# Kernel tuning notes

Hardware: AMD Instinct MI355X
Metric: run time of the kernel (lower is better)

Reference implementation:

```python
import jax, jax.numpy as jnp
import numpy as np

EPS = 1e-6
NUM_HEADS = 4


def setup_inputs() -> dict:
    key = jax.random.key(0)
    ks = jax.random.split(key, 7)
    B, C, H, W = 4, 128, 64, 64
    x = jax.random.normal(ks[0], (B, C, H, W), dtype=jnp.float32)
    norm_w = jnp.ones((C,), dtype=jnp.float32)
    norm_b = jnp.zeros((C,), dtype=jnp.float32)
    # 1x1 convs stored as [out_ch, in_ch] matrices
    qkv_w = jax.random.normal(ks[1], (3 * C, C), dtype=jnp.float32) / np.sqrt(C)
    qkv_b = jnp.zeros((3 * C,), dtype=jnp.float32)
    proj_w = jax.random.normal(ks[2], (C, C), dtype=jnp.float32) / np.sqrt(C)
    proj_b = jnp.zeros((C,), dtype=jnp.float32)
    return {"x": x, "norm_w": norm_w, "norm_b": norm_b,
            "qkv_w": qkv_w, "qkv_b": qkv_b, "proj_w": proj_w, "proj_b": proj_b}


def reference(x, norm_w, norm_b, qkv_w, qkv_b, proj_w, proj_b):
    B, C, H, W = x.shape
    nh = NUM_HEADS
    dh = C // nh
    N = H * W

    # ChannelLayerNorm: stats over channel dim per spatial position
    mean = jnp.mean(x, axis=1, keepdims=True)
    var = jnp.mean(jnp.square(x - mean), axis=1, keepdims=True)  # unbiased=False
    h = (x - mean) * jax.lax.rsqrt(var + EPS)
    h = h * norm_w[None, :, None, None] + norm_b[None, :, None, None]

    # qkv 1x1 conv -> [B, 3C, H, W]
    qkv = jnp.einsum('oc,bchw->bohw', qkv_w, h) + qkv_b[None, :, None, None]
    qkv = qkv.reshape(B, 3, nh, dh, N)
    q, k, v = qkv[:, 0], qkv[:, 1], qkv[:, 2]  # each [B, nh, dh, N]

    scale = dh ** -0.5
    attn = jnp.einsum('bhcn,bhcm->bhnm', q, k) * scale  # [B, nh, N, N]
    attn = jax.nn.softmax(attn, axis=-1)
    h = jnp.einsum('bhnm,bhcm->bhcn', attn, v)  # [B, nh, dh, N]
    h = h.reshape(B, C, H, W)

    h = jnp.einsum('oc,bchw->bohw', proj_w, h) + proj_b[None, :, None, None]
    return x + h
```

## Files before the change

kernel.cpp:

```cpp
#include <hip/hip_runtime.h>
#include <hip/hip_bf16.h>
#include <math.h>

#define BB 4
#define CC 128
#define NH 4
#define DH 32
#define NN 4096
#define OC3 (3*CC)

typedef __attribute__((ext_vector_type(8))) short short8;
typedef __attribute__((ext_vector_type(4))) short short4v;
typedef __attribute__((ext_vector_type(4))) float float4v;

__device__ inline short f2bf(float f) {
    unsigned u = __builtin_bit_cast(unsigned, f);
    u += 0x7FFF + ((u >> 16) & 1);
    return (short)(u >> 16);
}
__device__ inline unsigned pk2bf(float a, float b) {
    __hip_bfloat162 h = __float22bfloat162_rn(make_float2(a, b));
    unsigned u; __builtin_memcpy(&u, &h, 4);
    return u;
}
__device__ inline float bf2f(short s) {
    unsigned u = ((unsigned)(unsigned short)s) << 16;
    return __builtin_bit_cast(float, u);
}

#define HS 136
__global__ __launch_bounds__(512, 4) void lnqkv_kernel(
        const float* __restrict__ x, const float* __restrict__ nw,
        const float* __restrict__ nb, const float* __restrict__ qw,
        const float* __restrict__ qbias,
        short* __restrict__ qT, short* __restrict__ kT, short* __restrict__ vv) {
    __shared__ short hT[64 * HS];
    __shared__ float red[16][64];
    __shared__ float mrs[2][64];
    int t = threadIdx.x;
    int n0g = blockIdx.x * 64;
    int b = n0g >> 12, n0 = n0g & (NN - 1);
    int nl = t & 63, cq = t >> 6;

    const float* xp = x + ((size_t)b * CC + cq * 16) * NN + n0 + nl;
    float xv[16];
    float s = 0.f, ss = 0.f;
    #pragma unroll
    for (int j = 0; j < 16; ++j) {
        xv[j] = xp[(size_t)j * NN];
        s += xv[j]; ss += xv[j] * xv[j];
    }
    red[cq][nl] = s; red[cq + 8][nl] = ss;
    __syncthreads();
    if (t < 64) {
        float s8 = 0.f, q8 = 0.f;
        #pragma unroll
        for (int j = 0; j < 8; ++j) { s8 += red[j][t]; q8 += red[j + 8][t]; }
        float mean = s8 * (1.0f / CC);
        float var  = q8 * (1.0f / CC) - mean * mean;
        mrs[0][t] = mean;
        mrs[1][t] = rsqrtf(var + 1e-6f);
    }
    __syncthreads();
    {
        float mean = mrs[0][nl], rsv = mrs[1][nl];
        #pragma unroll
        for (int j = 0; j < 16; j += 8) {
            union { short8 v; unsigned u[4]; } z;
            #pragma unroll
            for (int k = 0; k < 4; ++k) {
                int c = cq * 16 + j + 2 * k;
                float h0 = (xv[j + 2 * k]     - mean) * rsv * nw[c]     + nb[c];
                float h1 = (xv[j + 2 * k + 1] - mean) * rsv * nw[c + 1] + nb[c + 1];
                z.u[k] = pk2bf(h0, h1);
            }
            *(short8*)&hT[nl * HS + cq * 16 + j] = z.v;
        }
    }
    __syncthreads();

    int w = t >> 6, lane = t & 63;
    int lg = lane >> 4, ln = lane & 15;
    int type = blockIdx.y;
    int ow = w * 16;
    const float* wp = qw + (size_t)(type * CC + ow + ln) * CC;
    float4v a0 = {0,0,0,0}, a1 = {0,0,0,0}, a2 = {0,0,0,0}, a3 = {0,0,0,0};
    #pragma unroll
    for (int cs = 0; cs < 4; ++cs) {
        float4 wa = *(const float4*)(wp + cs * 32 + lg * 8);
        float4 wb = *(const float4*)(wp + cs * 32 + lg * 8 + 4);
        union { short8 v; unsigned u[4]; } af;
        af.u[0] = pk2bf(wa.x, wa.y); af.u[1] = pk2bf(wa.z, wa.w);
        af.u[2] = pk2bf(wb.x, wb.y); af.u[3] = pk2bf(wb.z, wb.w);
        const short* hp = &hT[cs * 32 + lg * 8];
        a0 = __builtin_amdgcn_mfma_f32_16x16x32_bf16(af.v, *(const short8*)&hp[(0  + ln) * HS], a0, 0, 0, 0);
        a1 = __builtin_amdgcn_mfma_f32_16x16x32_bf16(af.v, *(const short8*)&hp[(16 + ln) * HS], a1, 0, 0, 0);
        a2 = __builtin_amdgcn_mfma_f32_16x16x32_bf16(af.v, *(const short8*)&hp[(32 + ln) * HS], a2, 0, 0, 0);
        a3 = __builtin_amdgcn_mfma_f32_16x16x32_bf16(af.v, *(const short8*)&hp[(48 + ln) * HS], a3, 0, 0, 0);
    }
    int r0g = type * CC + ow + lg * 4;
    float b0 = qbias[r0g], b1 = qbias[r0g + 1], b2 = qbias[r0g + 2], b3 = qbias[r0g + 3];
    int hh = ow >> 5;
    int cb = ow & 31;
    float4v* accs[4] = {&a0, &a1, &a2, &a3};
    if (type == 0) {
        const float qs = 0.1767766952966369f * 1.4426950408889634f;
        size_t rowbase = (size_t)(b * NH + hh) * NN + n0;
        #pragma unroll
        for (int nsub = 0; nsub < 4; ++nsub) {
            float4v av = *accs[nsub];
            union { short4v v; unsigned u[2]; } z;
            z.u[0] = pk2bf((av.x + b0) * qs, (av.y + b1) * qs);
            z.u[1] = pk2bf((av.z + b2) * qs, (av.w + b3) * qs);
            *(short4v*)&qT[(rowbase + nsub * 16 + ln) * DH + cb + lg * 4] = z.v;
        }
    } else if (type == 1) {
        size_t rowbase = (size_t)(b * NH + hh) * NN + n0;
        #pragma unroll
        for (int nsub = 0; nsub < 4; ++nsub) {
            float4v av = *accs[nsub];
            union { short4v v; unsigned u[2]; } z;
            z.u[0] = pk2bf(av.x + b0, av.y + b1);
            z.u[1] = pk2bf(av.z + b2, av.w + b3);
            *(short4v*)&kT[(rowbase + nsub * 16 + ln) * DH + cb + lg * 4] = z.v;
        }
    } else {
        size_t cbase = (size_t)((b * NH + hh) * DH + cb + lg * 4);
        #pragma unroll
        for (int nsub = 0; nsub < 4; ++nsub) {
            float4v av = *accs[nsub];
            size_t col = (size_t)n0 + nsub * 16 + ln;
            vv[(cbase + 0) * NN + col] = f2bf(av.x + b0);
            vv[(cbase + 1) * NN + col] = f2bf(av.y + b1);
            vv[(cbase + 2) * NN + col] = f2bf(av.z + b2);
            vv[(cbase + 3) * NN + col] = f2bf(av.w + b3);
        }
    }
}

#define PS 72
union __align__(16) FlashSh {
    short pt[8 * 4 * 16 * PS];
    struct { float mo[3][8][64][8]; float ml[3][8][64]; } m;
};
__global__ __launch_bounds__(512, 2) void flash_kernel(
        const short* __restrict__ qT, const short* __restrict__ kT,
        const short* __restrict__ vv, short* __restrict__ aoT) {
    __shared__ FlashSh sh;
    int blk = blockIdx.x;
    int bh = blk >> 5;
    int qb = blk & 31;
    int b = bh >> 2, hh = bh & 3;
    int n0 = qb * 128;
    int t = threadIdx.x, w = t >> 6, lane = t & 63;
    int lg = lane >> 4, ln = lane & 15;
    int qg = w & 1;
    int split = w >> 1;
    int swz = (ln & 3) << 2;

    const short* kbase = kT + (size_t)bh * NN * DH + lg * 8;
    const short* vb0 = vv + ((size_t)bh * DH + ln) * NN + lg * 8;
    const short* vb1 = vb0 + (size_t)16 * NN;

    short8 qf[4];
    #pragma unroll
    for (int j = 0; j < 4; ++j)
        qf[j] = *(const short8*)&qT[((size_t)bh * NN + n0 + (qg * 4 + j) * 16 + ln) * DH + lg * 8];

    float4v o0[4], o1[4];
    float ls[4];
    #pragma unroll
    for (int j = 0; j < 4; ++j) {
        o0[j] = (float4v){0,0,0,0}; o1[j] = (float4v){0,0,0,0}; ls[j] = 0.f;
    }
    short* ptw = &sh.pt[(w * 4) * 16 * PS];

    int mbeg = split * (NN / 4), mend = mbeg + NN / 4;
    for (int m0 = mbeg; m0 < mend; m0 += 64) {
        const short* kp = kbase + (size_t)m0 * DH;
        short8 k0 = *(const short8*)(kp + (size_t)(ln +  0) * DH);
        short8 k1 = *(const short8*)(kp + (size_t)(ln + 16) * DH);
        short8 k2 = *(const short8*)(kp + (size_t)(ln + 32) * DH);
        short8 k3 = *(const short8*)(kp + (size_t)(ln + 48) * DH);
        short8 v0 = *(const short8*)(vb0 + m0);
        short8 v1 = *(const short8*)(vb0 + m0 + 32);
        short8 v2 = *(const short8*)(vb1 + m0);
        short8 v3 = *(const short8*)(vb1 + m0 + 32);

        #pragma unroll
        for (int j = 0; j < 4; ++j) {
            float4v s0 = {0,0,0,0}, s1 = s0, s2 = s0, s3 = s0;
            s0 = __builtin_amdgcn_mfma_f32_16x16x32_bf16(k0, qf[j], s0, 0, 0, 0);
            s1 = __builtin_amdgcn_mfma_f32_16x16x32_bf16(k1, qf[j], s1, 0, 0, 0);
            s2 = __builtin_amdgcn_mfma_f32_16x16x32_bf16(k2, qf[j], s2, 0, 0, 0);
            s3 = __builtin_amdgcn_mfma_f32_16x16x32_bf16(k3, qf[j], s3, 0, 0, 0);
            short* ptj = ptw + j * 16 * PS;
            float lacc = 0.f;
            float4v* sv[4] = {&s0, &s1, &s2, &s3};
            #pragma unroll
            for (int jj = 0; jj < 4; ++jj) {
                float4v sj = *sv[jj];
                float p0 = __builtin_amdgcn_exp2f(sj.x);
                float p1 = __builtin_amdgcn_exp2f(sj.y);
                float p2 = __builtin_amdgcn_exp2f(sj.z);
                float p3 = __builtin_amdgcn_exp2f(sj.w);
                lacc += (p0 + p1) + (p2 + p3);
                union { short4v v; unsigned u[2]; } z;
                z.u[0] = pk2bf(p0, p1); z.u[1] = pk2bf(p2, p3);
                *(short4v*)&ptj[ln * PS + ((jj * 4 + lg) ^ swz) * 4] = z.v;
            }
            ls[j] += lacc;
        }

        #pragma unroll
        for (int j = 0; j < 4; ++j) {
            short* ptj = ptw + j * 16 * PS;
            short8 pb0 = *(const short8*)&ptj[ln * PS + ((2 * lg) ^ swz) * 4];
            short8 pb1 = *(const short8*)&ptj[ln * PS + ((8 + 2 * lg) ^ swz) * 4];
            o0[j] = __builtin_amdgcn_mfma_f32_16x16x32_bf16(v0, pb0, o0[j], 0, 0, 0);
            o1[j] = __builtin_amdgcn_mfma_f32_16x16x32_bf16(v2, pb0, o1[j], 0, 0, 0);
            o0[j] = __builtin_amdgcn_mfma_f32_16x16x32_bf16(v1, pb1, o0[j], 0, 0, 0);
            o1[j] = __builtin_amdgcn_mfma_f32_16x16x32_bf16(v3, pb1, o1[j], 0, 0, 0);
        }
    }

    __syncthreads();
    if (split > 0) {
        int si = split - 1;
        #pragma unroll
        for (int j = 0; j < 4; ++j) {
            int tid = qg * 4 + j;
            float* mp = &sh.m.mo[si][tid][lane][0];
            *(float4*)(mp + 0) = make_float4(o0[j].x, o0[j].y, o0[j].z, o0[j].w);
            *(float4*)(mp + 4) = make_float4(o1[j].x, o1[j].y, o1[j].z, o1[j].w);
            sh.m.ml[si][tid][lane] = ls[j];
        }
    }
    __syncthreads();
    if (split == 0) {
        #pragma unroll
        for (int j = 0; j < 4; ++j) {
            int tid = qg * 4 + j;
            #pragma unroll
            for (int si = 0; si < 3; ++si) {
                const float* mp = &sh.m.mo[si][tid][lane][0];
                float4 a0 = *(const float4*)(mp + 0);
                float4 a1 = *(const float4*)(mp + 4);
                o0[j].x += a0.x; o0[j].y += a0.y; o0[j].z += a0.z; o0[j].w += a0.w;
                o1[j].x += a1.x; o1[j].y += a1.y; o1[j].z += a1.z; o1[j].w += a1.w;
                ls[j] += sh.m.ml[si][tid][lane];
            }
            float lt = ls[j];
            lt += __shfl_xor(lt, 16, 64);
            lt += __shfl_xor(lt, 32, 64);
            float inv = 1.0f / lt;
            short* ap = aoT + ((size_t)b * NN + n0 + tid * 16 + ln) * CC + hh * DH;
            union { short4v v; unsigned u[2]; } z;
            z.u[0] = pk2bf(o0[j].x * inv, o0[j].y * inv);
            z.u[1] = pk2bf(o0[j].z * inv, o0[j].w * inv);
            *(short4v*)&ap[lg * 4] = z.v;
            z.u[0] = pk2bf(o1[j].x * inv, o1[j].y * inv);
            z.u[1] = pk2bf(o1[j].z * inv, o1[j].w * inv);
            *(short4v*)&ap[16 + lg * 4] = z.v;
        }
    }
}

__global__ __launch_bounds__(256) void proj_kernel(
        const short* __restrict__ aoT, const float* __restrict__ pw,
        const float* __restrict__ pb, const float* __restrict__ x,
        float* __restrict__ out) {
    int t = threadIdx.x;
    int n0g = blockIdx.x * 32;
    int b = n0g >> 12, n0 = n0g & (NN - 1);
    int o0 = blockIdx.y * 64;
    int wo = t >> 6, lane = t & 63;
    int lg = lane >> 4, ln = lane & 15;
    int ow = o0 + wo * 16;
    const float* wp = pw + (size_t)(ow + ln) * CC;
    const short* ap = aoT + (size_t)n0g * CC + lg * 8;
    float4v a0 = {0,0,0,0}, a1 = {0,0,0,0};
    #pragma unroll
    for (int cs = 0; cs < 4; ++cs) {
        float4 wa = *(const float4*)(wp + cs * 32 + lg * 8);
        float4 wb = *(const float4*)(wp + cs * 32 + lg * 8 + 4);
        union { short8 v; unsigned u[4]; } af;
        af.u[0] = pk2bf(wa.x, wa.y); af.u[1] = pk2bf(wa.z, wa.w);
        af.u[2] = pk2bf(wb.x, wb.y); af.u[3] = pk2bf(wb.z, wb.w);
        const short* hp = ap + cs * 32;
        a0 = __builtin_amdgcn_mfma_f32_16x16x32_bf16(af.v, *(const short8*)&hp[(size_t)(0  + ln) * CC], a0, 0, 0, 0);
        a1 = __builtin_amdgcn_mfma_f32_16x16x32_bf16(af.v, *(const short8*)&hp[(size_t)(16 + ln) * CC], a1, 0, 0, 0);
    }
    int r0 = ow + lg * 4;
    float b0 = pb[r0], b1 = pb[r0 + 1], b2 = pb[r0 + 2], b3 = pb[r0 + 3];
    const float* xbase = x   + ((size_t)b * CC + r0) * NN + n0 + ln;
    float*       obase = out + ((size_t)b * CC + r0) * NN + n0 + ln;
    float4v* accs[2] = {&a0, &a1};
    #pragma unroll
    for (int nsub = 0; nsub < 2; ++nsub) {
        float4v av = *accs[nsub];
        const float* xp = xbase + nsub * 16;
        float* op = obase + nsub * 16;
        op[(size_t)0 * NN] = av.x + b0 + xp[(size_t)0 * NN];
        op[(size_t)1 * NN] = av.y + b1 + xp[(size_t)1 * NN];
        op[(size_t)2 * NN] = av.z + b2 + xp[(size_t)2 * NN];
        op[(size_t)3 * NN] = av.w + b3 + xp[(size_t)3 * NN];
    }
}

extern "C" void kernel_launch(void* const* d_in, const int* in_sizes, int n_in,
                              void* d_out, int out_size, void* d_ws, size_t ws_size,
                              hipStream_t stream) {
    const float* x    = (const float*)d_in[0];
    const float* nw   = (const float*)d_in[1];
    const float* nb   = (const float*)d_in[2];
    const float* qkvw = (const float*)d_in[3];
    const float* qkvb = (const float*)d_in[4];
    const float* pw   = (const float*)d_in[5];
    const float* pb   = (const float*)d_in[6];
    float* out = (float*)d_out;

    short* qT  = (short*)d_ws;
    short* kT  = qT + (size_t)BB * NH * NN * DH;
    short* vv  = kT + (size_t)BB * NH * NN * DH;
    short* aoT = vv + (size_t)BB * NH * DH * NN;

    lnqkv_kernel<<<dim3(256, 3), 512, 0, stream>>>(x, nw, nb, qkvw, qkvb, qT, kT, vv);
    flash_kernel<<<dim3(512), 512, 0, stream>>>(qT, kT, vv, aoT);
    proj_kernel<<<dim3(512, 2), 256, 0, stream>>>(aoT, pw, pb, x, out);
}
```

Before: 147.2 us.

## Double-buffer K fragments in registers and drop P-tile LDS swizzle

Restructures the flash attention inner loop to prefetch the next 64-key K fragments into a second register set while computing the current tile, unrolling by two to ping-pong the buffers. It also removes the XOR swizzle on the P-tile LDS writes and reads, using plain padded offsets instead. The prefetch is meant to hide global load latency behind MFMA and exp work. The cost is extra VGPR pressure under the 512x2 launch bounds, and the unswizzled layout may bring LDS bank conflicts back.

After: 159.7 us. +8.5%, slower.

```diff
diff --git a/kernel.cpp b/kernel.cpp
--- a/kernel.cpp
+++ b/kernel.cpp
@@ -143,6 +143,61 @@
     short pt[8 * 4 * 16 * PS];
     struct { float mo[3][8][64][8]; float ml[3][8][64]; } m;
 };
+
+__device__ __forceinline__ void flash_step(
+        int m0, int mpf,
+        const short* __restrict__ kbase, const short* __restrict__ vb0,
+        const short* __restrict__ vb1,
+        int ln, int lg, const short8 (&qf)[4],
+        short8 (&kc)[4], short8 (&kn)[4],
+        float4v (&o0)[4], float4v (&o1)[4], float (&ls)[4], short* ptw) {
+    short8 v0 = *(const short8*)(vb0 + m0);
+    short8 v1 = *(const short8*)(vb0 + m0 + 32);
+    short8 v2 = *(const short8*)(vb1 + m0);
+    short8 v3 = *(const short8*)(vb1 + m0 + 32);
+    {
+        const short* kp = kbase + (size_t)mpf * DH;
+        kn[0] = *(const short8*)(kp + (size_t)(ln +  0) * DH);
+        kn[1] = *(const short8*)(kp + (size_t)(ln + 16) * DH);
+        kn[2] = *(const short8*)(kp + (size_t)(ln + 32) * DH);
+        kn[3] = *(const short8*)(kp + (size_t)(ln + 48) * DH);
+    }
+    #pragma unroll
+    for (int j = 0; j < 4; ++j) {
+        float4v s0 = {0,0,0,0}, s1 = s0, s2 = s0, s3 = s0;
+        s0 = __builtin_amdgcn_mfma_f32_16x16x32_bf16(kc[0], qf[j], s0, 0, 0, 0);
+        s1 = __builtin_amdgcn_mfma_f32_16x16x32_bf16(kc[1], qf[j], s1, 0, 0, 0);
+        s2 = __builtin_amdgcn_mfma_f32_16x16x32_bf16(kc[2], qf[j], s2, 0, 0, 0);
+        s3 = __builtin_amdgcn_mfma_f32_16x16x32_bf16(kc[3], qf[j], s3, 0, 0, 0);
+        short* ptj = ptw + j * 16 * PS;
+        float lacc = 0.f;
+        float4v* sv[4] = {&s0, &s1, &s2, &s3};
+        #pragma unroll
+        for (int jj = 0; jj < 4; ++jj) {
+            float4v sj = *sv[jj];
+            float p0 = __builtin_amdgcn_exp2f(sj.x);
+            float p1 = __builtin_amdgcn_exp2f(sj.y);
+            float p2 = __builtin_amdgcn_exp2f(sj.z);
+            float p3 = __builtin_amdgcn_exp2f(sj.w);
+            lacc += (p0 + p1) + (p2 + p3);
+            union { short4v v; unsigned u[2]; } z;
+            z.u[0] = pk2bf(p0, p1); z.u[1] = pk2bf(p2, p3);
+            *(short4v*)&ptj[ln * PS + jj * 16 + lg * 4] = z.v;
+        }
+        ls[j] += lacc;
+    }
+    #pragma unroll
+    for (int j = 0; j < 4; ++j) {
+        short* ptj = ptw + j * 16 * PS;
+        short8 pb0 = *(const short8*)&ptj[ln * PS + 0  + lg * 8];
+        short8 pb1 = *(const short8*)&ptj[ln * PS + 32 + lg * 8];
+        o0[j] = __builtin_amdgcn_mfma_f32_16x16x32_bf16(v0, pb0, o0[j], 0, 0, 0);
+        o1[j] = __builtin_amdgcn_mfma_f32_16x16x32_bf16(v2, pb0, o1[j], 0, 0, 0);
+        o0[j] = __builtin_amdgcn_mfma_f32_16x16x32_bf16(v1, pb1, o0[j], 0, 0, 0);
+        o1[j] = __builtin_amdgcn_mfma_f32_16x16x32_bf16(v3, pb1, o1[j], 0, 0, 0);
+    }
+}
+
 __global__ __launch_bounds__(512, 2) void flash_kernel(
         const short* __restrict__ qT, const short* __restrict__ kT,
         const short* __restrict__ vv, short* __restrict__ aoT) {
@@ -156,7 +211,6 @@
     int lg = lane >> 4, ln = lane & 15;
     int qg = w & 1;
     int split = w >> 1;
-    int swz = (ln & 3) << 2;
 
     const short* kbase = kT + (size_t)bh * NN * DH + lg * 8;
     const short* vb0 = vv + ((size_t)bh * DH + ln) * NN + lg * 8;
@@ -176,52 +230,18 @@
     short* ptw = &sh.pt[(w * 4) * 16 * PS];
 
     int mbeg = split * (NN / 4), mend = mbeg + NN / 4;
-    for (int m0 = mbeg; m0 < mend; m0 += 64) {
-        const short* kp = kbase + (size_t)m0 * DH;
-        short8 k0 = *(const short8*)(kp + (size_t)(ln +  0) * DH);
-        short8 k1 = *(const short8*)(kp + (size_t)(ln + 16) * DH);
-        short8 k2 = *(const short8*)(kp + (size_t)(ln + 32) * DH);
-        short8 k3 = *(const short8*)(kp + (size_t)(ln + 48) * DH);
-        short8 v0 = *(const short8*)(vb0 + m0);
-        short8 v1 = *(const short8*)(vb0 + m0 + 32);
-        short8 v2 = *(const short8*)(vb1 + m0);
-        short8 v3 = *(const short8*)(vb1 + m0 + 32);
-
-        #pragma unroll
-        for (int j = 0; j < 4; ++j) {
-            float4v s0 = {0,0,0,0}, s1 = s0, s2 = s0, s3 = s0;
-            s0 = __builtin_amdgcn_mfma_f32_16x16x32_bf16(k0, qf[j], s0, 0, 0, 0);
-            s1 = __builtin_amdgcn_mfma_f32_16x16x32_bf16(k1, qf[j], s1, 0, 0, 0);
-            s2 = __builtin_amdgcn_mfma_f32_16x16x32_bf16(k2, qf[j], s2, 0, 0, 0);
-            s3 = __builtin_amdgcn_mfma_f32_16x16x32_bf16(k3, qf[j], s3, 0, 0, 0);
-            short* ptj = ptw + j * 16 * PS;
-            float lacc = 0.f;
-            float4v* sv[4] = {&s0, &s1, &s2, &s3};
-            #pragma unroll
-            for (int jj = 0; jj < 4; ++jj) {
-                float4v sj = *sv[jj];
-                float p0 = __builtin_amdgcn_exp2f(sj.x);
-                float p1 = __builtin_amdgcn_exp2f(sj.y);
-                float p2 = __builtin_amdgcn_exp2f(sj.z);
-                float p3 = __builtin_amdgcn_exp2f(sj.w);
-                lacc += (p0 + p1) + (p2 + p3);
-                union { short4v v; unsigned u[2]; } z;
-                z.u[0] = pk2bf(p0, p1); z.u[1] = pk2bf(p2, p3);
-                *(short4v*)&ptj[ln * PS + ((jj * 4 + lg) ^ swz) * 4] = z.v;
-            }
-            ls[j] += lacc;
-        }
-
-        #pragma unroll
-        for (int j = 0; j < 4; ++j) {
-            short* ptj = ptw + j * 16 * PS;
-            short8 pb0 = *(const short8*)&ptj[ln * PS + ((2 * lg) ^ swz) * 4];
-            short8 pb1 = *(const short8*)&ptj[ln * PS + ((8 + 2 * lg) ^ swz) * 4];
-            o0[j] = __builtin_amdgcn_mfma_f32_16x16x32_bf16(v0, pb0, o0[j], 0, 0, 0);
-            o1[j] = __builtin_amdgcn_mfma_f32_16x16x32_bf16(v2, pb0, o1[j], 0, 0, 0);
-            o0[j] = __builtin_amdgcn_mfma_f32_16x16x32_bf16(v1, pb1, o0[j], 0, 0, 0);
-            o1[j] = __builtin_amdgcn_mfma_f32_16x16x32_bf16(v3, pb1, o1[j], 0, 0, 0);
-        }
+    short8 ka[4], kb[4];
+    {
+        const short* kp = kbase + (size_t)mbeg * DH;
+        ka[0] = *(const short8*)(kp + (size_t)(ln +  0) * DH);
+        ka[1] = *(const short8*)(kp + (size_t)(ln + 16) * DH);
+        ka[2] = *(const short8*)(kp + (size_t)(ln + 32) * DH);
+        ka[3] = *(const short8*)(kp + (size_t)(ln + 48) * DH);
+    }
+    for (int m0 = mbeg; m0 < mend; m0 += 128) {
+        int mp2 = (m0 + 128 < mend) ? m0 + 128 : mbeg;
+        flash_step(m0,      m0 + 64, kbase, vb0, vb1, ln, lg, qf, ka, kb, o0, o1, ls, ptw);
+        flash_step(m0 + 64, mp2,     kbase, vb0, vb1, ln, lg, qf, kb, ka, o0, o1, ls, ptw);
     }
 
     __syncthreads();
```
